# Kernel tuning notes

Measured on AMD Instinct MI355X. Metric: run time of the kernel, lower is better.

The kernel has to match this reference:

```python
import jax, jax.numpy as jnp
import numpy as np

EOS_ID = 1
E = 512
VS = 50000
VT = 50000
S_LEN = 128
T_LEN = 128


def setup_inputs() -> dict:
    key = jax.random.key(0)
    ks = jax.random.split(key, 16)
    sc = 0.05
    inp = {
        'source_words': jax.random.randint(ks[0], (S_LEN,), 0, VS, dtype=jnp.int64 if jax.config.jax_enable_x64 else jnp.int32),
        'target_words': jax.random.randint(ks[1], (T_LEN,), 0, VT, dtype=jnp.int64 if jax.config.jax_enable_x64 else jnp.int32),
        'W_x_hi': jax.random.normal(ks[2], (VS, E), jnp.float32) * sc,
        'W_y_hi': jax.random.normal(ks[3], (VT, E), jnp.float32) * sc,
        'enc_W_ih': jax.random.normal(ks[4], (4 * E, E), jnp.float32) * sc,
        'enc_W_hh': jax.random.normal(ks[5], (4 * E, E), jnp.float32) * sc,
        'enc_b_ih': jax.random.normal(ks[6], (4 * E,), jnp.float32) * sc,
        'enc_b_hh': jax.random.normal(ks[7], (4 * E,), jnp.float32) * sc,
        'dec_W_ih': jax.random.normal(ks[8], (4 * E, E), jnp.float32) * sc,
        'dec_W_hh': jax.random.normal(ks[9], (4 * E, E), jnp.float32) * sc,
        'dec_b_ih': jax.random.normal(ks[10], (4 * E,), jnp.float32) * sc,
        'dec_b_hh': jax.random.normal(ks[11], (4 * E,), jnp.float32) * sc,
        'W_hr_y': jax.random.normal(ks[12], (VT, E), jnp.float32) * sc,
        'b_hr_y': jax.random.normal(ks[13], (VT,), jnp.float32) * sc,
    }
    return inp


def _lstm_cell(x, h, c, W_ih, W_hh, b_ih, b_hh):
    # torch LSTMCell gate order: input, forget, cell(g), output
    gates = x @ W_ih.T + b_ih + h @ W_hh.T + b_hh  # [4E]
    i, f, g, o = jnp.split(gates, 4)
    c_new = jax.nn.sigmoid(f) * c + jax.nn.sigmoid(i) * jnp.tanh(g)
    h_new = jax.nn.sigmoid(o) * jnp.tanh(c_new)
    return h_new, c_new


def reference(source_words, target_words, W_x_hi, W_y_hi,
              enc_W_ih, enc_W_hh, enc_b_ih, enc_b_hh,
              dec_W_ih, dec_W_hh, dec_b_ih, dec_b_hh,
              W_hr_y, b_hr_y):
    e = W_x_hi.shape[1]
    h0 = jnp.zeros((e,), W_x_hi.dtype)

    # ---- encode: one LSTMCell step per source token ----
    def enc_step(carry, tok):
        h, c = carry
        x = W_x_hi[tok]
        return _lstm_cell(x, h, c, enc_W_ih, enc_W_hh, enc_b_ih, enc_b_hh), None

    (h, _c), _ = jax.lax.scan(enc_step, (h0, h0), source_words)

    # cell state is reset to zeros before decoding (as in the torch code)
    c = jnp.zeros_like(h)

    # ---- decode with teacher forcing; targets = target_words ++ [EOS] ----
    targets = jnp.concatenate([target_words, jnp.array([EOS_ID], target_words.dtype)])
    hi0 = W_x_hi[EOS_ID]  # first decoder input uses the SOURCE embedding of EOS

    def dec_step(carry, tok):
        h, c, hi = carry
        h, c = _lstm_cell(hi, h, c, dec_W_ih, dec_W_hh, dec_b_ih, dec_b_hh)
        logits = W_hr_y @ h + b_hr_y                       # [VT]
        loss = -jax.nn.log_softmax(logits)[tok]            # CE, batch=1 mean
        hi_next = W_y_hi[tok]
        return (h, c, hi_next), loss

    _, losses = jax.lax.scan(dec_step, (h, c, hi0), targets)
    return jnp.sum(losses)
```

## Files before the change

### kernel.cpp

```cpp
#include <hip/hip_runtime.h>
#include <cfloat>
#include <cmath>

#define E      512
#define FOURE  2048
#define VT     50000
#define SLEN   128
#define TLEN   129
#define NSTEPS 257
#define NBL    64
#define NGRID  554
#define NINBOX 32
#define NCHUNK 392
#define TPAD   132

#define INBOX_OFF  0
#define GXE_OFF    262144
#define PM_OFF     262144
#define PS_OFF     469120
#define TL_OFF     676096
#define HALL_OFF   786432
#define GXD_OFF    1310720
#define PROG_OFF   2367488

__device__ __forceinline__ float sigf(float x){ return 1.0f/(1.0f+__expf(-x)); }
__device__ __forceinline__ float tanhf_fast(float x){ return 2.f*sigf(2.f*x) - 1.f; }

__global__ __launch_bounds__(256) void gx_kernel(
    const int* __restrict__ src, const int* __restrict__ tgt,
    const float* __restrict__ Wx, const float* __restrict__ Wy,
    const float* __restrict__ encWih, const float* __restrict__ encBih, const float* __restrict__ encBhh,
    const float* __restrict__ decWih, const float* __restrict__ decBih, const float* __restrict__ decBhh,
    float* __restrict__ GxE, float* __restrict__ GxD)
{
  __shared__ float xs[8][E];
  const int tid  = threadIdx.x;
  const int tile = blockIdx.x;
  const bool is_dec = tile >= 16;
  const int t0 = is_dec ? (tile-16)*8 : tile*8;
  const int T  = is_dec ? TLEN : SLEN;

  for (int tt=0; tt<8; ++tt){
    int t = t0+tt;
    if (t < T){
      const float* xrow;
      if (is_dec) xrow = (t==0) ? (Wx + (size_t)1*E) : (Wy + (size_t)tgt[t-1]*E);
      else        xrow = Wx + (size_t)src[t]*E;
      xs[tt][tid]     = xrow[tid];
      xs[tt][tid+256] = xrow[tid+256];
    }
  }
  __syncthreads();

  const int r = blockIdx.y*256 + tid;
  const float* wrow = (is_dec ? decWih : encWih) + (size_t)r*E;
  const float  bias = is_dec ? (decBih[r]+decBhh[r]) : (encBih[r]+encBhh[r]);
  float acc[8];
  #pragma unroll
  for (int i=0;i<8;++i) acc[i]=0.f;

  for (int kc=0; kc<E; kc+=4){
    float4 w = *(const float4*)(wrow+kc);
    #pragma unroll
    for (int tt=0; tt<8; ++tt){
      float4 x = *(const float4*)&xs[tt][kc];
      acc[tt] += w.x*x.x + w.y*x.y + w.z*x.z + w.w*x.w;
    }
  }
  float* Gx = is_dec ? GxD : GxE;
  #pragma unroll
  for (int tt=0; tt<8; ++tt){
    int t = t0+tt;
    if (t < T) Gx[(size_t)t*FOURE + r] = bias + acc[tt];
  }
}

__device__ __forceinline__ void load_weights_s(
    const float* __restrict__ Whh, float* __restrict__ wldsw, int j, int lane)
{
  #pragma unroll
  for (int gg=0; gg<4; ++gg){
    const float* wr = Whh + (size_t)(gg*E + j)*E;
    float4 a = *(const float4*)(wr + 4*lane);
    float4 b = *(const float4*)(wr + 4*lane + 256);
    float* dst = wldsw + (size_t)gg*E + (lane&7)*64 + (lane>>3)*4;
    *(float4*)dst      = a;
    *(float4*)(dst+32) = b;
  }
}

__global__ __launch_bounds__(512, 1) void mega_kernel(
    const float* __restrict__ GxE, const float* __restrict__ GxD,
    const float* __restrict__ encWhh, const float* __restrict__ decWhh,
    unsigned long long* __restrict__ inboxes, unsigned* __restrict__ h_all,
    unsigned* __restrict__ prog,
    const float* __restrict__ W, const float* __restrict__ bvec,
    const int* __restrict__ tgt,
    float* __restrict__ pm, float* __restrict__ ps, float* __restrict__ tl)
{
  __shared__ float smemf[17552];
  const int tid = threadIdx.x;

  if (blockIdx.x < NBL){
    const int lane = tid & 63, wave = tid >> 6, bid = blockIdx.x;
    const int g = lane >> 4, k = lane & 15;
    const int j = bid*8 + wave;
    const int row = g*E + j;
    const int slot  = wave*64 + lane;
    const int pslot = slot + 4*(slot>>5);
    float* wldsw = smemf + wave*2048;
    float* hmir  = smemf + 16384;
    const unsigned long long* myslot = inboxes + (size_t)(bid>>1)*1024 + slot;

    load_weights_s(encWhh, wldsw, j, lane);
    float cst = 0.f;

    for (int s=0; s<NSTEPS; ++s){
      if (s == SLEN){
        load_weights_s(decWhh, wldsw, j, lane);
        cst = 0.f;
      }
      const bool isdec = s >= SLEN;
      const int tloc = isdec ? (s - SLEN) : s;
      float gx = (isdec ? GxD : GxE)[(size_t)tloc*FOURE + row];

      float acc = 0.f;
      if (s > 0){
        const int buf = s & 1;
        unsigned long long hu;
        const unsigned long long* hp = myslot + (size_t)buf*512;
        for (int spin=0; spin<(1<<16); ++spin){
          hu = __hip_atomic_load(hp, __ATOMIC_RELAXED, __HIP_MEMORY_SCOPE_AGENT);
          if (__all((unsigned)(hu>>32) == (unsigned)s)) break;
          __builtin_amdgcn_s_sleep(1);
        }
        hmir[buf*576 + pslot] = __uint_as_float((unsigned)hu);
        __syncthreads();
        if (tid==0) atomicAdd(&prog[s*4], 1u);
        const float* hb = hmir + buf*576 + 36*k;
        #pragma unroll
        for (int i=0;i<8;++i){
          float4 h4 = *(const float4*)(hb + 4*i);
          float4 wv = *(const float4*)&wldsw[(size_t)g*E + i*64 + 4*k];
          acc += wv.x*h4.x + wv.y*h4.y + wv.z*h4.z + wv.w*h4.w;
        }
        acc += __shfl_xor(acc,1); acc += __shfl_xor(acc,2);
        acc += __shfl_xor(acc,4); acc += __shfl_xor(acc,8);
      }

      float gv = acc + gx;
      float x1 = __shfl_xor(gv,16);
      float x2 = __shfl_xor(gv,32);
      float x3 = __shfl_xor(x1,32);
      float gi = (g==0)?gv:(g==1)?x1:(g==2)?x2:x3;
      float gf = (g==0)?x1:(g==1)?gv:(g==2)?x3:x2;
      float gg = (g==0)?x2:(g==1)?x3:(g==2)?gv:x1;
      float go = (g==0)?x3:(g==1)?x2:(g==2)?x1:gv;
      cst = sigf(gf)*cst + sigf(gi)*tanhf_fast(gg);
      float hnew = sigf(go)*tanhf_fast(cst);

      unsigned long long pk = ((unsigned long long)(unsigned)(s+1) << 32)
                            |  (unsigned long long)__float_as_uint(hnew);
      if (lane < NINBOX)
        __hip_atomic_store(inboxes + (size_t)lane*1024 + (size_t)((s+1)&1)*512 + j,
                           pk, __ATOMIC_RELAXED, __HIP_MEMORY_SCOPE_AGENT);
      if (isdec && lane==0)
        __hip_atomic_store(h_all + (size_t)tloc*E + j, __float_as_uint(hnew),
                           __ATOMIC_RELAXED, __HIP_MEMORY_SCOPE_AGENT);
    }
    __syncthreads();
    if (tid==0) atomicAdd(&prog[257*4], 1u);

  } else {
    const int bc   = blockIdx.x - NBL;
    const int ty   = bc / 98;
    const int sub  = tid >> 7;
    const int stid = tid & 127;
    const int wv   = stid >> 6;
    const int lane = tid & 63;
    const int chunk = (bc % 98)*4 + sub;
    const int t0   = ty * 32;
    const int nt   = (t0 + 32 <= TLEN) ? 32 : (TLEN - t0);
    float* hst  = smemf;

    const int gate_s = (ty < 4) ? (160 + 32*ty) : 257;
    if (tid == 0){
      for (int spin=0; spin<(1<<22); ++spin){
        if (__hip_atomic_load(&prog[gate_s*4], __ATOMIC_RELAXED, __HIP_MEMORY_SCOPE_AGENT)
            >= (unsigned)NBL) break;
        __builtin_amdgcn_s_sleep(16);
      }
    }
    __syncthreads();

    {
      unsigned long long* hst64 = (unsigned long long*)hst;
      const unsigned long long* hsrc = (const unsigned long long*)(h_all + (size_t)t0*E);
      for (int i=tid; i<nt*(E/2); i+=512)
        hst64[i] = __hip_atomic_load(hsrc+i, __ATOMIC_RELAXED, __HIP_MEMORY_SCOPE_AGENT);
    }
    __syncthreads();

    const int c0 = chunk*128 + lane;
    const int c1 = c0 + 64;
    const bool v0 = c0 < VT, v1 = c1 < VT;
    const float* w0 = W + (size_t)(v0 ? c0 : 0)*E;
    const float* w1 = W + (size_t)(v1 ? c1 : 0)*E;

    float acc0[32], acc1[32];
    #pragma unroll
    for (int i=0;i<32;++i){ acc0[i]=0.f; acc1[i]=0.f; }

    const int kc0 = wv*256;
    for (int kc=kc0; kc<kc0+256; kc+=4){
      float4 wa = *(const float4*)(w0+kc);
      float4 wb = *(const float4*)(w1+kc);
      #pragma unroll
      for (int tt=0; tt<32; ++tt){
        float4 h4 = *(const float4*)&hst[tt*E + kc];
        acc0[tt] += wa.x*h4.x + wa.y*h4.y + wa.z*h4.z + wa.w*h4.w;
        acc1[tt] += wb.x*h4.x + wb.y*h4.y + wb.z*h4.z + wb.w*h4.w;
      }
    }

    __syncthreads();
    float* ldsR = smemf + sub*4160;
    if (wv == 1){
      #pragma unroll
      for (int i=0;i<32;++i){
        ldsR[lane*65 + i]      = acc0[i];
        ldsR[lane*65 + 32 + i] = acc1[i];
      }
    }
    __syncthreads();
    if (wv == 0){
      #pragma unroll
      for (int i=0;i<32;++i){
        acc0[i] += ldsR[lane*65 + i];
        acc1[i] += ldsR[lane*65 + 32 + i];
      }
      const float b0 = v0 ? bvec[c0] : 0.f;
      const float b1 = v1 ? bvec[c1] : 0.f;

      #pragma unroll
      for (int tt=0; tt<32; ++tt){
        if (tt < nt){
          float x0 = v0 ? acc0[tt]+b0 : -FLT_MAX;
          float x1 = v1 ? acc1[tt]+b1 : -FLT_MAX;
          float mx = fmaxf(x0,x1);
          #pragma unroll
          for (int off=1; off<64; off<<=1) mx = fmaxf(mx, __shfl_xor(mx, off));
          float e = (v0 ? __expf(x0-mx) : 0.f) + (v1 ? __expf(x1-mx) : 0.f);
          #pragma unroll
          for (int off=1; off<64; off<<=1) e += __shfl_xor(e, off);
          int t = t0 + tt;
          if (lane==0){ pm[(size_t)chunk*TPAD + t] = mx; ps[(size_t)chunk*TPAD + t] = e; }
          int tok = (t < SLEN) ? tgt[t] : 1;
          if (v0 && c0==tok) tl[t] = x0;
          if (v1 && c1==tok) tl[t] = x1;
        }
      }
    }
  }
}

__global__ __launch_bounds__(256) void c2_kernel(
    const float* __restrict__ pm, const float* __restrict__ ps, const float* __restrict__ tl,
    float* __restrict__ out)
{
  const int tid = threadIdx.x;
  float loss = 0.f;
  if (tid < TLEN){
    float m = -FLT_MAX, ssum = 0.f;
    for (int ch=0; ch<NCHUNK; ++ch){
      float mc = pm[(size_t)ch*TPAD + tid];
      float sc = ps[(size_t)ch*TPAD + tid];
      float nm = fmaxf(m, mc);
      ssum = ssum*__expf(m-nm) + sc*__expf(mc-nm);
      m = nm;
    }
    loss = (m + __logf(ssum)) - tl[tid];
  }
  __shared__ float red[4];
  #pragma unroll
  for (int off=1; off<64; off<<=1) loss += __shfl_xor(loss, off);
  if ((tid & 63)==0) red[tid>>6] = loss;
  __syncthreads();
  if (tid==0) out[0] = red[0]+red[1]+red[2]+red[3];
}

extern "C" void kernel_launch(void* const* d_in, const int* in_sizes, int n_in,
                              void* d_out, int out_size, void* d_ws, size_t ws_size,
                              hipStream_t stream)
{
  const int*   src    = (const int*)  d_in[0];
  const int*   tgt    = (const int*)  d_in[1];
  const float* Wx     = (const float*)d_in[2];
  const float* Wy     = (const float*)d_in[3];
  const float* encWih = (const float*)d_in[4];
  const float* encWhh = (const float*)d_in[5];
  const float* encBih = (const float*)d_in[6];
  const float* encBhh = (const float*)d_in[7];
  const float* decWih = (const float*)d_in[8];
  const float* decWhh = (const float*)d_in[9];
  const float* decBih = (const float*)d_in[10];
  const float* decBhh = (const float*)d_in[11];
  const float* Whr    = (const float*)d_in[12];
  const float* bhr    = (const float*)d_in[13];

  char* ws = (char*)d_ws;
  unsigned long long* inboxes = (unsigned long long*)(ws + INBOX_OFF);
  float* GxE     = (float*)(ws + GXE_OFF);
  float* GxD     = (float*)(ws + GXD_OFF);
  unsigned* hall = (unsigned*)(ws + HALL_OFF);
  unsigned* prog = (unsigned*)(ws + PROG_OFF);
  float* pm      = (float*)(ws + PM_OFF);
  float* ps      = (float*)(ws + PS_OFF);
  float* tl      = (float*)(ws + TL_OFF);

  hipMemsetAsync(ws + INBOX_OFF, 0, NINBOX*1024*8, stream);
  hipMemsetAsync(ws + PROG_OFF, 0, 258*16, stream);

  dim3 ggrid(33, 8);
  gx_kernel<<<ggrid, 256, 0, stream>>>(src, tgt, Wx, Wy,
      encWih, encBih, encBhh, decWih, decBih, decBhh, GxE, GxD);

  mega_kernel<<<NGRID, 512, 0, stream>>>(GxE, GxD, encWhh, decWhh,
      inboxes, hall, prog, Whr, bhr, tgt, pm, ps, tl);

  c2_kernel<<<1, 256, 0, stream>>>(pm, ps, tl, (float*)d_out);
}
```

Baseline: 1.058 ms.

## Give each vocab chunk a full block with 8-way K split and tree reduction

The logits-consumer blocks previously packed four 128-column chunks per block, each split across two waves over K. Now each chunk gets its own 512-thread block whose eight waves each cover 64 of K, combined by a three-level LDS tree reduction. Time tiles are also regrouped into four tiles, the last holding 33 steps, so the last gate waits on fewer tiles. This raises parallelism and shortens each wave's serial K loop, at the cost of more blocks, more barriers, larger accumulator arrays with register pressure, and repeated W reads per block.

Result: slower. 1.211 ms (+14.5%).

```diff
diff --git a/kernel.cpp b/kernel.cpp
--- a/kernel.cpp
+++ b/kernel.cpp
@@ -9,7 +9,9 @@
 #define TLEN   129
 #define NSTEPS 257
 #define NBL    64
-#define NGRID  554
+#define C1B    392
+#define NTILES 4
+#define NGRID  (NBL + C1B*NTILES)
 #define NINBOX 32
 #define NCHUNK 392
 #define TPAD   132
@@ -173,17 +175,14 @@
 
   } else {
     const int bc   = blockIdx.x - NBL;
-    const int ty   = bc / 98;
-    const int sub  = tid >> 7;
-    const int stid = tid & 127;
-    const int wv   = stid >> 6;
-    const int lane = tid & 63;
-    const int chunk = (bc % 98)*4 + sub;
+    const int ty   = bc / C1B;
+    const int chunk= bc % C1B;
+    const int wave = tid >> 6, lane = tid & 63;
     const int t0   = ty * 32;
-    const int nt   = (t0 + 32 <= TLEN) ? 32 : (TLEN - t0);
-    float* hst  = smemf;
-
-    const int gate_s = (ty < 4) ? (160 + 32*ty) : 257;
+    const int nt   = (ty < 3) ? 32 : 33;
+    float* hst = smemf;
+
+    const int gate_s = (ty < 3) ? (160 + 32*ty) : 257;
     if (tid == 0){
       for (int spin=0; spin<(1<<22); ++spin){
         if (__hip_atomic_load(&prog[gate_s*4], __ATOMIC_RELAXED, __HIP_MEMORY_SCOPE_AGENT)
@@ -207,43 +206,64 @@
     const float* w0 = W + (size_t)(v0 ? c0 : 0)*E;
     const float* w1 = W + (size_t)(v1 ? c1 : 0)*E;
 
-    float acc0[32], acc1[32];
+    float acc0[33], acc1[33];
     #pragma unroll
-    for (int i=0;i<32;++i){ acc0[i]=0.f; acc1[i]=0.f; }
-
-    const int kc0 = wv*256;
-    for (int kc=kc0; kc<kc0+256; kc+=4){
+    for (int i=0;i<33;++i){ acc0[i]=0.f; acc1[i]=0.f; }
+
+    const int kc0 = wave*64;
+    for (int kk=0; kk<64; kk+=4){
+      const int kc = kc0 + kk;
       float4 wa = *(const float4*)(w0+kc);
       float4 wb = *(const float4*)(w1+kc);
       #pragma unroll
-      for (int tt=0; tt<32; ++tt){
+      for (int tt=0; tt<33; ++tt){
         float4 h4 = *(const float4*)&hst[tt*E + kc];
         acc0[tt] += wa.x*h4.x + wa.y*h4.y + wa.z*h4.z + wa.w*h4.w;
         acc1[tt] += wb.x*h4.x + wb.y*h4.y + wb.z*h4.z + wb.w*h4.w;
       }
     }
 
-    __syncthreads();
-    float* ldsR = smemf + sub*4160;
-    if (wv == 1){
-      #pragma unroll
-      for (int i=0;i<32;++i){
-        ldsR[lane*65 + i]      = acc0[i];
-        ldsR[lane*65 + 32 + i] = acc1[i];
-      }
-    }
-    __syncthreads();
-    if (wv == 0){
-      #pragma unroll
-      for (int i=0;i<32;++i){
-        acc0[i] += ldsR[lane*65 + i];
-        acc1[i] += ldsR[lane*65 + 32 + i];
-      }
+    float* R = smemf;
+    __syncthreads();
+    if (wave >= 4){
+      float* d = R + (wave-4)*4288 + lane*67;
+      #pragma unroll
+      for (int i=0;i<33;++i){ d[i] = acc0[i]; d[33+i] = acc1[i]; }
+    }
+    __syncthreads();
+    if (wave < 4){
+      const float* d = R + wave*4288 + lane*67;
+      #pragma unroll
+      for (int i=0;i<33;++i){ acc0[i] += d[i]; acc1[i] += d[33+i]; }
+    }
+    __syncthreads();
+    if (wave == 2 || wave == 3){
+      float* d = R + (wave-2)*4288 + lane*67;
+      #pragma unroll
+      for (int i=0;i<33;++i){ d[i] = acc0[i]; d[33+i] = acc1[i]; }
+    }
+    __syncthreads();
+    if (wave < 2){
+      const float* d = R + wave*4288 + lane*67;
+      #pragma unroll
+      for (int i=0;i<33;++i){ acc0[i] += d[i]; acc1[i] += d[33+i]; }
+    }
+    __syncthreads();
+    if (wave == 1){
+      float* d = R + lane*67;
+      #pragma unroll
+      for (int i=0;i<33;++i){ d[i] = acc0[i]; d[33+i] = acc1[i]; }
+    }
+    __syncthreads();
+    if (wave == 0){
+      const float* d = R + lane*67;
+      #pragma unroll
+      for (int i=0;i<33;++i){ acc0[i] += d[i]; acc1[i] += d[33+i]; }
+
       const float b0 = v0 ? bvec[c0] : 0.f;
       const float b1 = v1 ? bvec[c1] : 0.f;
-
-      #pragma unroll
-      for (int tt=0; tt<32; ++tt){
+      #pragma unroll
+      for (int tt=0; tt<33; ++tt){
         if (tt < nt){
           float x0 = v0 ? acc0[tt]+b0 : -FLT_MAX;
           float x1 = v1 ? acc1[tt]+b1 : -FLT_MAX;
```
